# Optimization experiments

Hardware: AMD Instinct MI355X
Metric: run time of the kernel (lower is better)

Reference implementation:

```python
import jax, jax.numpy as jnp
import numpy as np

B, S, HID = 1, 2048, 2880
H, KV, D = 64, 8, 64
WINDOW = 128
SCALE = D ** -0.5
NEG_INF = jnp.float32(-1e30)


def _rope_cos_sin():
    # realistic RoPE tables over full head_dim (HF rotate_half convention)
    inv_freq = 1.0 / (10000.0 ** (np.arange(0, D, 2, dtype=np.float32) / D))
    t = np.arange(S, dtype=np.float32)
    freqs = np.outer(t, inv_freq)                      # [S, D/2]
    emb = np.concatenate([freqs, freqs], axis=-1)      # [S, D]
    return jnp.asarray(np.cos(emb))[None], jnp.asarray(np.sin(emb))[None]


def setup_inputs() -> dict:
    key = jax.random.key(0)
    ks = jax.random.split(key, 10)
    cos, sin = _rope_cos_sin()
    sd = lambda fan_in: 1.0 / np.sqrt(fan_in)
    return {
        "hidden_states": jax.random.normal(ks[0], (B, S, HID), jnp.float32),
        "cos": cos, "sin": sin,
        "Wq": jax.random.normal(ks[1], (HID, H * D), jnp.float32) * sd(HID),
        "bq": jax.random.normal(ks[2], (H * D,), jnp.float32) * 0.02,
        "Wk": jax.random.normal(ks[3], (HID, KV * D), jnp.float32) * sd(HID),
        "bk": jax.random.normal(ks[4], (KV * D,), jnp.float32) * 0.02,
        "Wv": jax.random.normal(ks[5], (HID, KV * D), jnp.float32) * sd(HID),
        "bv": jax.random.normal(ks[6], (KV * D,), jnp.float32) * 0.02,
        "Wo": jax.random.normal(ks[7], (H * D, HID), jnp.float32) * sd(H * D),
        "bo": jax.random.normal(ks[8], (HID,), jnp.float32) * 0.02,
        "sinks": jax.random.normal(ks[9], (H,), jnp.float32),
    }


def _rotate_half(x):
    x1, x2 = jnp.split(x, 2, axis=-1)
    return jnp.concatenate([-x2, x1], axis=-1)


def _forward(hidden_states, cos, sin, Wq, bq, Wk, bk, Wv, bv, Wo, bo, sinks):
    q = (hidden_states @ Wq + bq).reshape(B, S, H, D)
    k = (hidden_states @ Wk + bk).reshape(B, S, KV, D)
    v = (hidden_states @ Wv + bv).reshape(B, S, KV, D)
    # RoPE with explicit cos/sin, unsqueeze at head dim (bsnd layout)
    c, s = cos[:, :, None, :], sin[:, :, None, :]
    q = q * c + _rotate_half(q) * s
    k = k * c + _rotate_half(k) * s
    # GQA: expand kv heads to match query heads
    k = jnp.repeat(k, H // KV, axis=2)
    v = jnp.repeat(v, H // KV, axis=2)
    scores = jnp.einsum("bqhd,bkhd->bhqk", q, k) * SCALE  # [B,H,S,S]
    i = jnp.arange(S)[:, None]
    j = jnp.arange(S)[None, :]
    allowed = (j <= i) & (j > i - WINDOW)                  # causal + sliding window
    scores = jnp.where(allowed, scores, NEG_INF)
    # sink-augmented softmax: sinks act as an extra logit per head, dropped after norm
    m = jnp.maximum(scores.max(axis=-1), sinks[None, :, None])  # [B,H,S]
    p = jnp.exp(scores - m[..., None])                      # [B,H,S,S]
    denom = p.sum(axis=-1) + jnp.exp(sinks[None, :, None] - m)  # [B,H,S]
    attn = jnp.einsum("bhqk,bkhd->bqhd", p, v) / denom.transpose(0, 2, 1)[..., None]
    return attn.reshape(B, S, H * D) @ Wo + bo


def reference(hidden_states, cos, sin, Wq, bq, Wk, bk, Wv, bv, Wo, bo, sinks):
    return _forward(hidden_states, cos, sin, Wq, bq, Wk, bk, Wv, bv, Wo, bo, sinks)
```

## Files before the change

kernel.cpp:

```cpp
#include <hip/hip_runtime.h>

typedef unsigned short u16;
typedef __bf16 bf16x8 __attribute__((ext_vector_type(8)));
typedef float f32x4 __attribute__((ext_vector_type(4)));

constexpr int SEQ = 2048;
constexpr int HIDN = 2880;
constexpr int NQKV = 5120;
constexpr float SCALE = 0.125f;
constexpr float NEG_INF = -1e30f;

#define ASM_VMCNT4()  asm volatile("s_waitcnt vmcnt(4)" ::: "memory")
#define ASM_VMCNT0()  asm volatile("s_waitcnt vmcnt(0)" ::: "memory")
#define ASM_LGKM0()   asm volatile("s_waitcnt lgkmcnt(0)" ::: "memory")
#define ASM_BARRIER() asm volatile("s_barrier" ::: "memory")

__device__ __forceinline__ u16 f2bf(float f) {
  unsigned int u = __builtin_bit_cast(unsigned int, f);
  u += 0x7FFFu + ((u >> 16) & 1u);
  return (u16)(u >> 16);
}
__device__ __forceinline__ float bf2f(u16 h) {
  unsigned int u = ((unsigned int)h) << 16;
  return __builtin_bit_cast(float, u);
}
__device__ __forceinline__ void async_load16(const void* g, void* l) {
  __builtin_amdgcn_global_load_lds(
      (const __attribute__((address_space(1))) unsigned int*)g,
      (__attribute__((address_space(3))) unsigned int*)l, 16, 0, 0);
}

__global__ __launch_bounds__(256) void conv_f2b(const float* __restrict__ in,
                                                u16* __restrict__ out, long n4) {
  long i = (long)blockIdx.x * 256 + threadIdx.x;
  if (i >= n4) return;
  float4 v = ((const float4*)in)[i];
  u16 o0 = f2bf(v.x), o1 = f2bf(v.y), o2 = f2bf(v.z), o3 = f2bf(v.w);
  out[i * 4 + 0] = o0; out[i * 4 + 1] = o1; out[i * 4 + 2] = o2; out[i * 4 + 3] = o3;
}

__global__ __launch_bounds__(256) void transpose_f2b(const float* __restrict__ in,
                                                     u16* __restrict__ out,
                                                     int R, int C, int ostride) {
  __shared__ float tile[32][33];
  int c0 = blockIdx.x * 32, r0 = blockIdx.y * 32;
  int tx = threadIdx.x & 31, ty = threadIdx.x >> 5;
#pragma unroll
  for (int i = 0; i < 32; i += 8)
    tile[ty + i][tx] = in[(long)(r0 + ty + i) * C + c0 + tx];
  __syncthreads();
#pragma unroll
  for (int i = 0; i < 32; i += 8)
    out[(long)(c0 + ty + i) * ostride + r0 + tx] = f2bf(tile[tx][ty + i]);
}

__global__ __launch_bounds__(256) void concat_bias(const float* bq, const float* bk,
                                                   const float* bv, float* out) {
  int t = blockIdx.x * 256 + threadIdx.x;
  if (t < 4096) out[t] = bq[t];
  else if (t < 4608) out[t] = bk[t - 4096];
  else if (t < 5120) out[t] = bv[t - 4608];
}

template <bool OUT_BF16>
__global__ __launch_bounds__(256, 3) void gemm_pipe(const u16* __restrict__ A,
                                                    const u16* __restrict__ B,
                                                    const float* __restrict__ bias,
                                                    void* __restrict__ Cout,
                                                    int M, int N, int K) {
  __shared__ u16 As[3][128 * 32];
  __shared__ u16 Bs[3][128 * 32];
  const int tid = threadIdx.x;
  const int wid = tid >> 6, lane = tid & 63;
  const int lr = lane & 15, lk = lane >> 4;
  const int wm = wid >> 1, wn = wid & 1;

  const int gm = gridDim.x;
  int nwg = gm * gridDim.y;
  int bid = blockIdx.y * gm + blockIdx.x;
  int q8 = nwg >> 3, r8 = nwg & 7;
  int xcd = bid & 7, seq = bid >> 3;
  int swz = (xcd < r8 ? xcd * (q8 + 1) : r8 * (q8 + 1) + (xcd - r8) * q8) + seq;
  const long brow = (long)(swz % gm) * 128;
  const long bcol = (long)(swz / gm) * 128;

  const int c0 = wid * 128 + lane;
  const int c1 = c0 + 64;
  const int r0s = c0 >> 2, k0s = ((c0 & 3) ^ ((r0s >> 1) & 3)) * 8;
  const int r1s = c1 >> 2, k1s = ((c1 & 3) ^ ((r1s >> 1) & 3)) * 8;
  const u16* Asrc0 = A + (brow + r0s) * (long)K + k0s;
  const u16* Asrc1 = A + (brow + r1s) * (long)K + k1s;
  const u16* Bsrc0 = B + (bcol + r0s) * (long)K + k0s;
  const u16* Bsrc1 = B + (bcol + r1s) * (long)K + k1s;
  char* AsB = (char*)&As[0][0];
  char* BsB = (char*)&Bs[0][0];

  auto stage = [&](int kt, int bufi) {
    long ko = (long)kt * 32;
    char* la = AsB + bufi * 8192;
    char* lb = BsB + bufi * 8192;
    async_load16(Asrc0 + ko, la + c0 * 16);
    async_load16(Bsrc0 + ko, lb + c0 * 16);
    async_load16(Asrc1 + ko, la + c1 * 16);
    async_load16(Bsrc1 + ko, lb + c1 * 16);
  };

  const int phys = (lk ^ ((lr >> 1) & 3)) << 4;
  const int aoff0 = (wm * 64 + lr) * 64 + phys;
  const int boff0 = (wn * 64 + lr) * 64 + phys;

  f32x4 acc[4][4] = {};
  const int nk = K >> 5;

  stage(0, 0);
  if (nk > 1) stage(1, 1);

  int b = 0, sb = 2;
  for (int kt = 0; kt < nk; ++kt) {
    if (kt + 1 < nk) { ASM_VMCNT4(); } else { ASM_VMCNT0(); }
    ASM_BARRIER();
    __builtin_amdgcn_sched_barrier(0);
    if (kt + 2 < nk) stage(kt + 2, sb);
    char* Ab_ = AsB + b * 8192;
    char* Bb_ = BsB + b * 8192;
    bf16x8 af[4], bfr[4];
#pragma unroll
    for (int m = 0; m < 4; ++m) af[m] = *(const bf16x8*)(Ab_ + aoff0 + m * 1024);
#pragma unroll
    for (int n = 0; n < 4; ++n) bfr[n] = *(const bf16x8*)(Bb_ + boff0 + n * 1024);
    ASM_LGKM0();
    __builtin_amdgcn_sched_barrier(0);
    __builtin_amdgcn_s_setprio(1);
#pragma unroll
    for (int m = 0; m < 4; ++m)
#pragma unroll
      for (int n = 0; n < 4; ++n)
        acc[m][n] = __builtin_amdgcn_mfma_f32_16x16x32_bf16(af[m], bfr[n], acc[m][n], 0, 0, 0);
    __builtin_amdgcn_s_setprio(0);
    b = (b == 2) ? 0 : b + 1;
    sb = (sb == 2) ? 0 : sb + 1;
  }

#pragma unroll
  for (int m = 0; m < 4; ++m) {
    long row = brow + wm * 64 + m * 16 + lk * 4;
#pragma unroll
    for (int n = 0; n < 4; ++n) {
      long col = bcol + wn * 64 + n * 16 + lr;
      if (col < N) {
        float bv = bias[col];
#pragma unroll
        for (int r = 0; r < 4; ++r) {
          float v = acc[m][n][r] + bv;
          if (OUT_BF16) ((u16*)Cout)[(row + r) * (long)N + col] = f2bf(v);
          else          ((float*)Cout)[(row + r) * (long)N + col] = v;
        }
      }
    }
  }
}

__global__ __launch_bounds__(256) void rope_kernel(u16* __restrict__ QKV,
                                                   const float* __restrict__ cosb,
                                                   const float* __restrict__ sinb) {
  long idx = (long)blockIdx.x * 256 + threadIdx.x;
  if (idx >= (long)SEQ * 72 * 32) return;
  int d = idx & 31;
  int h = (int)((idx >> 5) % 72);
  int s = (int)(idx / (72 * 32));
  int col = (h < 64) ? h * 64 : 4096 + (h - 64) * 64;
  u16* p = QKV + (long)s * NQKV + col;
  float x1 = bf2f(p[d]), x2 = bf2f(p[d + 32]);
  float c = cosb[s * 64 + d], sn = sinb[s * 64 + d];
  p[d]      = f2bf(x1 * c - x2 * sn);
  p[d + 32] = f2bf(x2 * c + x1 * sn);
}

__global__ __launch_bounds__(256, 1) void attn_kernel(const u16* __restrict__ QKV,
                                                      const float* __restrict__ sinks,
                                                      u16* __restrict__ Oa) {
  __shared__ u16 Ks[64 * 64];
  __shared__ u16 Vt[64 * 64];
  __shared__ u16 Ps[4][64 * 72];
  const int tid = threadIdx.x, wid = tid >> 6, lane = tid & 63;
  const int lr = lane & 15, lk = lane >> 4;
  const int i0 = blockIdx.x * 64;
  const int h = blockIdx.y * 4 + wid;
  const int g = h >> 3;

  bf16x8 qf[4][2];
#pragma unroll
  for (int m = 0; m < 4; ++m)
#pragma unroll
    for (int kc = 0; kc < 2; ++kc)
      qf[m][kc] = *(const bf16x8*)&QKV[(long)(i0 + m * 16 + lr) * NQKV + h * 64 + kc * 32 + lk * 8];

  const float sinkh = sinks[h];
  float mrun[4][4], lrun[4][4];
  f32x4 oacc[4][4] = {};
#pragma unroll
  for (int m = 0; m < 4; ++m)
#pragma unroll
    for (int r = 0; r < 4; ++r) { mrun[m][r] = sinkh; lrun[m][r] = 0.f; }

  const int jb0 = (i0 >= 128) ? (i0 - 128) : 0;
  for (int jb = jb0; jb <= i0; jb += 64) {
#pragma unroll
    for (int i = 0; i < 2; ++i) {
      int c = wid * 128 + i * 64 + lane;
      int row = c >> 3, sp = c & 7;
      int ssrc = sp ^ (row & 7);
      async_load16(QKV + (long)(jb + row) * NQKV + 4096 + g * 64 + ssrc * 8,
                   ((char*)Ks) + c * 16);
    }
    {
      int j0 = (tid & 31) * 2, d0 = (tid >> 5) * 8;
      const u16* vp = QKV + (long)(jb + j0) * NQKV + 4608 + g * 64 + d0;
      int4 rv0 = *(const int4*)vp;
      int4 rv1 = *(const int4*)(vp + NQKV);
      const u16* a0 = (const u16*)&rv0;
      const u16* a1 = (const u16*)&rv1;
#pragma unroll
      for (int e = 0; e < 8; ++e) {
        int d = d0 + e;
        unsigned val = (unsigned)a0[e] | ((unsigned)a1[e] << 16);
        int byt = d * 128 + ((((j0 >> 3) ^ (d & 7)) << 4)) + ((j0 & 7) * 2);
        *(unsigned*)((char*)Vt + byt) = val;
      }
    }
    __syncthreads();

    f32x4 sf[4][4] = {};
    __builtin_amdgcn_s_setprio(1);
#pragma unroll
    for (int kc = 0; kc < 2; ++kc) {
      bf16x8 kf[4];
#pragma unroll
      for (int cf = 0; cf < 4; ++cf) {
        int row = cf * 16 + lr;
        kf[cf] = *(const bf16x8*)((const char*)Ks + row * 128 + (((kc * 4 + lk) ^ (lr & 7)) << 4));
      }
#pragma unroll
      for (int m = 0; m < 4; ++m)
#pragma unroll
        for (int cf = 0; cf < 4; ++cf)
          sf[m][cf] = __builtin_amdgcn_mfma_f32_16x16x32_bf16(qf[m][kc], kf[cf], sf[m][cf], 0, 0, 0);
    }
    __builtin_amdgcn_s_setprio(0);

#pragma unroll
    for (int m = 0; m < 4; ++m) {
      float rmax[4];
#pragma unroll
      for (int r = 0; r < 4; ++r) {
        int i = i0 + m * 16 + lk * 4 + r;
        float mx = NEG_INF;
#pragma unroll
        for (int cf = 0; cf < 4; ++cf) {
          int j = jb + cf * 16 + lr;
          float v = sf[m][cf][r] * SCALE;
          bool ok = (j <= i) && (j > i - 128);
          v = ok ? v : NEG_INF;
          sf[m][cf][r] = v;
          mx = fmaxf(mx, v);
        }
#pragma unroll
        for (int off = 1; off < 16; off <<= 1) mx = fmaxf(mx, __shfl_xor(mx, off, 64));
        rmax[r] = mx;
      }
#pragma unroll
      for (int r = 0; r < 4; ++r) {
        float mnew = fmaxf(mrun[m][r], rmax[r]);
        float corr = __expf(mrun[m][r] - mnew);
        mrun[m][r] = mnew;
        float rsum = 0.f;
#pragma unroll
        for (int cf = 0; cf < 4; ++cf) {
          float p = __expf(sf[m][cf][r] - mnew);
          sf[m][cf][r] = p;
          rsum += p;
        }
#pragma unroll
        for (int off = 1; off < 16; off <<= 1) rsum += __shfl_xor(rsum, off, 64);
        lrun[m][r] = lrun[m][r] * corr + rsum;
#pragma unroll
        for (int dn = 0; dn < 4; ++dn) oacc[m][dn][r] *= corr;
      }
    }

#pragma unroll
    for (int m = 0; m < 4; ++m)
#pragma unroll
      for (int cf = 0; cf < 4; ++cf)
#pragma unroll
        for (int r = 0; r < 4; ++r)
          Ps[wid][(m * 16 + lk * 4 + r) * 72 + cf * 16 + lr] = f2bf(sf[m][cf][r]);
    __syncthreads();

    __builtin_amdgcn_s_setprio(1);
#pragma unroll
    for (int kc = 0; kc < 2; ++kc) {
      bf16x8 pf[4], vf[4];
#pragma unroll
      for (int m = 0; m < 4; ++m)
        pf[m] = *(const bf16x8*)&Ps[wid][(m * 16 + lr) * 72 + kc * 32 + lk * 8];
#pragma unroll
      for (int dn = 0; dn < 4; ++dn) {
        int row = dn * 16 + lr;
        vf[dn] = *(const bf16x8*)((const char*)Vt + row * 128 + (((kc * 4 + lk) ^ (lr & 7)) << 4));
      }
#pragma unroll
      for (int m = 0; m < 4; ++m)
#pragma unroll
        for (int dn = 0; dn < 4; ++dn)
          oacc[m][dn] = __builtin_amdgcn_mfma_f32_16x16x32_bf16(pf[m], vf[dn], oacc[m][dn], 0, 0, 0);
    }
    __builtin_amdgcn_s_setprio(0);
    __syncthreads();
  }

#pragma unroll
  for (int m = 0; m < 4; ++m)
#pragma unroll
    for (int r = 0; r < 4; ++r) {
      float denom = lrun[m][r] + __expf(sinkh - mrun[m][r]);
      float inv = 1.f / denom;
      long row = i0 + m * 16 + lk * 4 + r;
#pragma unroll
      for (int dn = 0; dn < 4; ++dn)
        Oa[row * 4096 + h * 64 + dn * 16 + lr] = f2bf(oacc[m][dn][r] * inv);
    }
}

extern "C" void kernel_launch(void* const* d_in, const int* in_sizes, int n_in,
                              void* d_out, int out_size, void* d_ws, size_t ws_size,
                              hipStream_t stream) {
  const float* X    = (const float*)d_in[0];
  const float* cosb = (const float*)d_in[1];
  const float* sinb = (const float*)d_in[2];
  const float* Wq   = (const float*)d_in[3];
  const float* bq   = (const float*)d_in[4];
  const float* Wk   = (const float*)d_in[5];
  const float* bk   = (const float*)d_in[6];
  const float* Wv   = (const float*)d_in[7];
  const float* bv   = (const float*)d_in[8];
  const float* Wo   = (const float*)d_in[9];
  const float* bo   = (const float*)d_in[10];
  const float* sinks = (const float*)d_in[11];

  char* ws = (char*)d_ws;
  size_t off = 0;
  auto alloc = [&](size_t bytes) -> void* {
    void* p = ws + off;
    off += (bytes + 255) & ~(size_t)255;
    return p;
  };
  u16*   Xb    = (u16*)alloc((size_t)SEQ * HIDN * 2);
  u16*   Wqkv  = (u16*)alloc((size_t)NQKV * HIDN * 2);
  u16*   Wot   = (u16*)alloc((size_t)2944 * 4096 * 2);
  float* bqkv  = (float*)alloc((size_t)NQKV * 4);
  u16*   QKV   = (u16*)alloc((size_t)SEQ * NQKV * 2);
  u16*   Ab    = (u16*)alloc((size_t)SEQ * 4096 * 2);
  (void)ws_size; (void)in_sizes; (void)n_in; (void)out_size;

  conv_f2b<<<(SEQ * HIDN / 4 + 255) / 256, 256, 0, stream>>>(X, Xb, (long)SEQ * HIDN / 4);
  transpose_f2b<<<dim3(4096 / 32, HIDN / 32), 256, 0, stream>>>(Wq, Wqkv, HIDN, 4096, HIDN);
  transpose_f2b<<<dim3(512 / 32, HIDN / 32), 256, 0, stream>>>(Wk, Wqkv + (size_t)4096 * HIDN, HIDN, 512, HIDN);
  transpose_f2b<<<dim3(512 / 32, HIDN / 32), 256, 0, stream>>>(Wv, Wqkv + (size_t)4608 * HIDN, HIDN, 512, HIDN);
  transpose_f2b<<<dim3(HIDN / 32, 4096 / 32), 256, 0, stream>>>(Wo, Wot, 4096, HIDN, 4096);
  concat_bias<<<(NQKV + 255) / 256, 256, 0, stream>>>(bq, bk, bv, bqkv);
  gemm_pipe<true><<<dim3(SEQ / 128, NQKV / 128), 256, 0, stream>>>(Xb, Wqkv, bqkv, QKV, SEQ, NQKV, HIDN);
  rope_kernel<<<(int)(((long)SEQ * 72 * 32 + 255) / 256), 256, 0, stream>>>(QKV, cosb, sinb);
  attn_kernel<<<dim3(SEQ / 64, 64 / 4), 256, 0, stream>>>(QKV, sinks, Ab);
  gemm_pipe<false><<<dim3(SEQ / 128, (HIDN + 127) / 128), 256, 0, stream>>>(Ab, Wot, bo, d_out, SEQ, HIDN, 4096);
}
```

Before: 259.7 us.

## Replace GEMMs with larger 512-thread tiles and deeper LDS pipelining

Replaces the generic 128x128 GEMM with two specialized kernels. The QKV projection gets a 256x256 tile over 8 waves, with A fragments split into two halves to overlap LDS reads and MFMA. The output projection gets a 128x256 tile with a 4-stage prefetch ring. Hand-written ds_read_b128 is used, and the XOR swizzle on LDS is dropped, which may cause bank conflicts. The Wo transpose buffer is padded to 3072 columns so the tiles cover it.

After: 248.8 us. 4.2% less time.

```diff
diff --git a/kernel.cpp b/kernel.cpp
--- a/kernel.cpp
+++ b/kernel.cpp
@@ -10,10 +10,10 @@
 constexpr float SCALE = 0.125f;
 constexpr float NEG_INF = -1e30f;
 
-#define ASM_VMCNT4()  asm volatile("s_waitcnt vmcnt(4)" ::: "memory")
-#define ASM_VMCNT0()  asm volatile("s_waitcnt vmcnt(0)" ::: "memory")
+#define ASM_VMCNT(n)  asm volatile("s_waitcnt vmcnt(" #n ")" ::: "memory")
 #define ASM_LGKM0()   asm volatile("s_waitcnt lgkmcnt(0)" ::: "memory")
 #define ASM_BARRIER() asm volatile("s_barrier" ::: "memory")
+#define SCHEDBAR()    __builtin_amdgcn_sched_barrier(0)
 
 __device__ __forceinline__ u16 f2bf(float f) {
   unsigned int u = __builtin_bit_cast(unsigned int, f);
@@ -29,6 +29,12 @@
       (const __attribute__((address_space(1))) unsigned int*)g,
       (__attribute__((address_space(3))) unsigned int*)l, 16, 0, 0);
 }
+__device__ __forceinline__ f32x4 DSR(unsigned addr) {
+  f32x4 d;
+  asm volatile("ds_read_b128 %0, %1" : "=v"(d) : "v"(addr));
+  return d;
+}
+__device__ __forceinline__ bf16x8 asbf(f32x4 v) { return __builtin_bit_cast(bf16x8, v); }
 
 __global__ __launch_bounds__(256) void conv_f2b(const float* __restrict__ in,
                                                 u16* __restrict__ out, long n4) {
@@ -62,18 +68,109 @@
   else if (t < 5120) out[t] = bv[t - 4608];
 }
 
-template <bool OUT_BF16>
-__global__ __launch_bounds__(256, 3) void gemm_pipe(const u16* __restrict__ A,
-                                                    const u16* __restrict__ B,
-                                                    const float* __restrict__ bias,
-                                                    void* __restrict__ Cout,
-                                                    int M, int N, int K) {
-  __shared__ u16 As[3][128 * 32];
-  __shared__ u16 Bs[3][128 * 32];
-  const int tid = threadIdx.x;
-  const int wid = tid >> 6, lane = tid & 63;
+__global__ __launch_bounds__(512, 2) void gemm256(const u16* __restrict__ A,
+                                                  const u16* __restrict__ B,
+                                                  const float* __restrict__ bias,
+                                                  u16* __restrict__ C,
+                                                  int N, int K) {
+  __shared__ u16 lds[3 * 16384];
+  const int tid = threadIdx.x, wid = tid >> 6, lane = tid & 63;
   const int lr = lane & 15, lk = lane >> 4;
-  const int wm = wid >> 1, wn = wid & 1;
+  const int wm = wid >> 2, wn = wid & 3;
+
+  const int gm = gridDim.x;
+  int nwg = gm * gridDim.y;
+  int bid = blockIdx.y * gm + blockIdx.x;
+  int q8 = nwg >> 3, r8 = nwg & 7;
+  int xcd = bid & 7, seq = bid >> 3;
+  int swz = (xcd < r8 ? xcd * (q8 + 1) : r8 * (q8 + 1) + (xcd - r8) * q8) + seq;
+  const long brow = (long)(swz % gm) * 256;
+  const long bcol = (long)(swz / gm) * 256;
+  const int nkt = K >> 5;
+
+  const int cA0 = tid, cA1 = tid + 512;
+  const u16* Asrc0 = A + (brow + (cA0 >> 2)) * (long)K + (cA0 & 3) * 8;
+  const u16* Asrc1 = A + (brow + (cA1 >> 2)) * (long)K + (cA1 & 3) * 8;
+  const u16* Bsrc0 = B + (bcol + (cA0 >> 2)) * (long)K + (cA0 & 3) * 8;
+  const u16* Bsrc1 = B + (bcol + (cA1 >> 2)) * (long)K + (cA1 & 3) * 8;
+  char* L = (char*)lds;
+  auto stage = [&](int kt, int b) {
+    long ko = (long)kt * 32;
+    char* d = L + b * 32768;
+    async_load16(Asrc0 + ko, d + cA0 * 16);
+    async_load16(Asrc1 + ko, d + cA1 * 16);
+    async_load16(Bsrc0 + ko, d + 16384 + cA0 * 16);
+    async_load16(Bsrc1 + ko, d + 16384 + cA1 * 16);
+  };
+
+  const unsigned lds0 = (unsigned)(size_t)L;
+  const unsigned aoff = lds0 + (unsigned)((wm * 128 + lr) * 64 + lk * 16);
+  const unsigned boff = lds0 + 16384u + (unsigned)((wn * 64 + lr) * 64 + lk * 16);
+
+  f32x4 acc[8][4] = {};
+  stage(0, 0);
+  stage(1, 1);
+  ASM_VMCNT(4);
+  ASM_BARRIER();
+
+  int b = 0;
+  for (int t = 0; t < nkt; ++t) {
+    const unsigned ab = aoff + b * 32768u;
+    const unsigned bb = boff + b * 32768u;
+    f32x4 afr[4], bfr[4];
+#pragma unroll
+    for (int m = 0; m < 4; ++m) afr[m] = DSR(ab + m * 1024u);
+#pragma unroll
+    for (int n = 0; n < 4; ++n) bfr[n] = DSR(bb + n * 1024u);
+    if (t + 2 < nkt) stage(t + 2, b == 0 ? 2 : b - 1);
+    ASM_LGKM0(); SCHEDBAR();
+    __builtin_amdgcn_s_setprio(1);
+#pragma unroll
+    for (int m = 0; m < 4; ++m)
+#pragma unroll
+      for (int n = 0; n < 4; ++n)
+        acc[m][n] = __builtin_amdgcn_mfma_f32_16x16x32_bf16(asbf(afr[m]), asbf(bfr[n]), acc[m][n], 0, 0, 0);
+    __builtin_amdgcn_s_setprio(0);
+    f32x4 afr2[4];
+#pragma unroll
+    for (int m = 0; m < 4; ++m) afr2[m] = DSR(ab + (m + 4) * 1024u);
+    if (t + 2 < nkt) { ASM_VMCNT(4); } else { ASM_VMCNT(0); }
+    ASM_BARRIER();
+    ASM_LGKM0(); SCHEDBAR();
+    __builtin_amdgcn_s_setprio(1);
+#pragma unroll
+    for (int m = 0; m < 4; ++m)
+#pragma unroll
+      for (int n = 0; n < 4; ++n)
+        acc[m + 4][n] = __builtin_amdgcn_mfma_f32_16x16x32_bf16(asbf(afr2[m]), asbf(bfr[n]), acc[m + 4][n], 0, 0, 0);
+    __builtin_amdgcn_s_setprio(0);
+    ASM_BARRIER();
+    b = (b == 2) ? 0 : b + 1;
+  }
+
+#pragma unroll
+  for (int m = 0; m < 8; ++m) {
+    long row = brow + wm * 128 + m * 16 + lk * 4;
+#pragma unroll
+    for (int n = 0; n < 4; ++n) {
+      long col = bcol + wn * 64 + n * 16 + lr;
+      float bv = bias[col];
+#pragma unroll
+      for (int r = 0; r < 4; ++r)
+        C[(row + r) * (long)N + col] = f2bf(acc[m][n][r] + bv);
+    }
+  }
+}
+
+__global__ __launch_bounds__(512, 2) void gemm128(const u16* __restrict__ A,
+                                                  const u16* __restrict__ B,
+                                                  const float* __restrict__ bias,
+                                                  float* __restrict__ C,
+                                                  int N, int K) {
+  __shared__ u16 lds[4 * 12288];
+  const int tid = threadIdx.x, wid = tid >> 6, lane = tid & 63;
+  const int lr = lane & 15, lk = lane >> 4;
+  const int wm = wid >> 2, wn = wid & 3;
 
   const int gm = gridDim.x;
   int nwg = gm * gridDim.y;
@@ -82,63 +179,56 @@
   int xcd = bid & 7, seq = bid >> 3;
   int swz = (xcd < r8 ? xcd * (q8 + 1) : r8 * (q8 + 1) + (xcd - r8) * q8) + seq;
   const long brow = (long)(swz % gm) * 128;
-  const long bcol = (long)(swz / gm) * 128;
-
-  const int c0 = wid * 128 + lane;
-  const int c1 = c0 + 64;
-  const int r0s = c0 >> 2, k0s = ((c0 & 3) ^ ((r0s >> 1) & 3)) * 8;
-  const int r1s = c1 >> 2, k1s = ((c1 & 3) ^ ((r1s >> 1) & 3)) * 8;
-  const u16* Asrc0 = A + (brow + r0s) * (long)K + k0s;
-  const u16* Asrc1 = A + (brow + r1s) * (long)K + k1s;
-  const u16* Bsrc0 = B + (bcol + r0s) * (long)K + k0s;
-  const u16* Bsrc1 = B + (bcol + r1s) * (long)K + k1s;
-  char* AsB = (char*)&As[0][0];
-  char* BsB = (char*)&Bs[0][0];
-
-  auto stage = [&](int kt, int bufi) {
+  const long bcol = (long)(swz / gm) * 256;
+  const int nkt = K >> 5;
+
+  const int cB0 = tid, cB1 = tid + 512;
+  const u16* AsrcP = A + (brow + (tid >> 2)) * (long)K + (tid & 3) * 8;
+  const u16* Bsrc0 = B + (bcol + (cB0 >> 2)) * (long)K + (cB0 & 3) * 8;
+  const u16* Bsrc1 = B + (bcol + (cB1 >> 2)) * (long)K + (cB1 & 3) * 8;
+  char* L = (char*)lds;
+  auto stage = [&](int kt, int b) {
     long ko = (long)kt * 32;
-    char* la = AsB + bufi * 8192;
-    char* lb = BsB + bufi * 8192;
-    async_load16(Asrc0 + ko, la + c0 * 16);
-    async_load16(Bsrc0 + ko, lb + c0 * 16);
-    async_load16(Asrc1 + ko, la + c1 * 16);
-    async_load16(Bsrc1 + ko, lb + c1 * 16);
+    char* d = L + b * 24576;
+    async_load16(AsrcP + ko, d + tid * 16);
+    async_load16(Bsrc0 + ko, d + 8192 + cB0 * 16);
+    async_load16(Bsrc1 + ko, d + 8192 + cB1 * 16);
   };
 
-  const int phys = (lk ^ ((lr >> 1) & 3)) << 4;
-  const int aoff0 = (wm * 64 + lr) * 64 + phys;
-  const int boff0 = (wn * 64 + lr) * 64 + phys;
+  const unsigned lds0 = (unsigned)(size_t)L;
+  const unsigned aoff = lds0 + (unsigned)((wm * 64 + lr) * 64 + lk * 16);
+  const unsigned boff = lds0 + 8192u + (unsigned)((wn * 64 + lr) * 64 + lk * 16);
 
   f32x4 acc[4][4] = {};
-  const int nk = K >> 5;
-
   stage(0, 0);
-  if (nk > 1) stage(1, 1);
-
-  int b = 0, sb = 2;
-  for (int kt = 0; kt < nk; ++kt) {
-    if (kt + 1 < nk) { ASM_VMCNT4(); } else { ASM_VMCNT0(); }
+  stage(1, 1);
+  stage(2, 2);
+  ASM_VMCNT(6);
+  ASM_BARRIER();
+
+  for (int t = 0; t < nkt; ++t) {
+    const int b = t & 3;
+    const unsigned ab = aoff + b * 24576u;
+    const unsigned bb = boff + b * 24576u;
+    f32x4 afr[4], bfr[4];
+#pragma unroll
+    for (int m = 0; m < 4; ++m) afr[m] = DSR(ab + m * 1024u);
+#pragma unroll
+    for (int n = 0; n < 4; ++n) bfr[n] = DSR(bb + n * 1024u);
+    if (t + 3 < nkt) stage(t + 3, (t + 3) & 3);
+    if (t + 3 < nkt)      { ASM_VMCNT(6); }
+    else if (t + 2 < nkt) { ASM_VMCNT(3); }
+    else                  { ASM_VMCNT(0); }
     ASM_BARRIER();
-    __builtin_amdgcn_sched_barrier(0);
-    if (kt + 2 < nk) stage(kt + 2, sb);
-    char* Ab_ = AsB + b * 8192;
-    char* Bb_ = BsB + b * 8192;
-    bf16x8 af[4], bfr[4];
-#pragma unroll
-    for (int m = 0; m < 4; ++m) af[m] = *(const bf16x8*)(Ab_ + aoff0 + m * 1024);
-#pragma unroll
-    for (int n = 0; n < 4; ++n) bfr[n] = *(const bf16x8*)(Bb_ + boff0 + n * 1024);
-    ASM_LGKM0();
-    __builtin_amdgcn_sched_barrier(0);
+    ASM_LGKM0(); SCHEDBAR();
     __builtin_amdgcn_s_setprio(1);
 #pragma unroll
     for (int m = 0; m < 4; ++m)
 #pragma unroll
       for (int n = 0; n < 4; ++n)
-        acc[m][n] = __builtin_amdgcn_mfma_f32_16x16x32_bf16(af[m], bfr[n], acc[m][n], 0, 0, 0);
+        acc[m][n] = __builtin_amdgcn_mfma_f32_16x16x32_bf16(asbf(afr[m]), asbf(bfr[n]), acc[m][n], 0, 0, 0);
     __builtin_amdgcn_s_setprio(0);
-    b = (b == 2) ? 0 : b + 1;
-    sb = (sb == 2) ? 0 : sb + 1;
+    ASM_BARRIER();
   }
 
 #pragma unroll
@@ -150,11 +240,8 @@
       if (col < N) {
         float bv = bias[col];
 #pragma unroll
-        for (int r = 0; r < 4; ++r) {
-          float v = acc[m][n][r] + bv;
-          if (OUT_BF16) ((u16*)Cout)[(row + r) * (long)N + col] = f2bf(v);
-          else          ((float*)Cout)[(row + r) * (long)N + col] = v;
-        }
+        for (int r = 0; r < 4; ++r)
+          C[(row + r) * (long)N + col] = acc[m][n][r] + bv;
       }
     }
   }
@@ -357,7 +444,7 @@
   };
   u16*   Xb    = (u16*)alloc((size_t)SEQ * HIDN * 2);
   u16*   Wqkv  = (u16*)alloc((size_t)NQKV * HIDN * 2);
-  u16*   Wot   = (u16*)alloc((size_t)2944 * 4096 * 2);
+  u16*   Wot   = (u16*)alloc((size_t)3072 * 4096 * 2);
   float* bqkv  = (float*)alloc((size_t)NQKV * 4);
   u16*   QKV   = (u16*)alloc((size_t)SEQ * NQKV * 2);
   u16*   Ab    = (u16*)alloc((size_t)SEQ * 4096 * 2);
@@ -369,8 +456,8 @@
   transpose_f2b<<<dim3(512 / 32, HIDN / 32), 256, 0, stream>>>(Wv, Wqkv + (size_t)4608 * HIDN, HIDN, 512, HIDN);
   transpose_f2b<<<dim3(HIDN / 32, 4096 / 32), 256, 0, stream>>>(Wo, Wot, 4096, HIDN, 4096);
   concat_bias<<<(NQKV + 255) / 256, 256, 0, stream>>>(bq, bk, bv, bqkv);
-  gemm_pipe<true><<<dim3(SEQ / 128, NQKV / 128), 256, 0, stream>>>(Xb, Wqkv, bqkv, QKV, SEQ, NQKV, HIDN);
+  gemm256<<<dim3(SEQ / 256, NQKV / 256), 512, 0, stream>>>(Xb, Wqkv, bqkv, QKV, NQKV, HIDN);
   rope_kernel<<<(int)(((long)SEQ * 72 * 32 + 255) / 256), 256, 0, stream>>>(QKV, cosb, sinb);
   attn_kernel<<<dim3(SEQ / 64, 64 / 4), 256, 0, stream>>>(QKV, sinks, Ab);
-  gemm_pipe<false><<<dim3(SEQ / 128, (HIDN + 127) / 128), 256, 0, stream>>>(Ab, Wot, bo, d_out, SEQ, HIDN, 4096);
-}
+  gemm128<<<dim3(SEQ / 128, 3072 / 256), 512, 0, stream>>>(Ab, Wot, bo, (float*)d_out, HIDN, 4096);
+}
```

## Widen GEMM tiles to 128x256 with split LDS reads and MFMA halves

Applied to the files above, without the earlier changes.

Replaces the 128x128 GEMM with a 128x256 tile kernel in which each of the four waves owns a 128x64 slice. That doubles the A-fragment reuse per B fragment and cuts redundant A traffic. The LDS fragment reads are issued as inline ds_read_b128 and split in two, so the first half of the MFMAs can start under a partial lgkmcnt wait while the rest of the reads complete. The output-projection weight buffer is padded to 3072 rows to fit the wider tile, and the stores stay guarded by col<N. The cost is fewer workgroups (192–320 on a 256-CU part), lower occupancy (2 blocks per CU instead of 3) and more LDS per block, which may leave CUs underused.

Measured after the change: 262.7 us. No clear change (+1.1%).

```diff
diff --git a/kernel.cpp b/kernel.cpp
--- a/kernel.cpp
+++ b/kernel.cpp
@@ -10,10 +10,10 @@
 constexpr float SCALE = 0.125f;
 constexpr float NEG_INF = -1e30f;
 
-#define ASM_VMCNT4()  asm volatile("s_waitcnt vmcnt(4)" ::: "memory")
-#define ASM_VMCNT0()  asm volatile("s_waitcnt vmcnt(0)" ::: "memory")
-#define ASM_LGKM0()   asm volatile("s_waitcnt lgkmcnt(0)" ::: "memory")
+#define ASM_VMCNT(n)  asm volatile("s_waitcnt vmcnt(" #n ")" ::: "memory")
+#define ASM_LGKM(n)   asm volatile("s_waitcnt lgkmcnt(" #n ")" ::: "memory")
 #define ASM_BARRIER() asm volatile("s_barrier" ::: "memory")
+#define SCHEDBAR()    __builtin_amdgcn_sched_barrier(0)
 
 __device__ __forceinline__ u16 f2bf(float f) {
   unsigned int u = __builtin_bit_cast(unsigned int, f);
@@ -29,6 +29,12 @@
       (const __attribute__((address_space(1))) unsigned int*)g,
       (__attribute__((address_space(3))) unsigned int*)l, 16, 0, 0);
 }
+__device__ __forceinline__ f32x4 DSR(unsigned addr) {
+  f32x4 d;
+  asm volatile("ds_read_b128 %0, %1" : "=v"(d) : "v"(addr));
+  return d;
+}
+__device__ __forceinline__ bf16x8 asbf(f32x4 v) { return __builtin_bit_cast(bf16x8, v); }
 
 __global__ __launch_bounds__(256) void conv_f2b(const float* __restrict__ in,
                                                 u16* __restrict__ out, long n4) {
@@ -63,17 +69,14 @@
 }
 
 template <bool OUT_BF16>
-__global__ __launch_bounds__(256, 3) void gemm_pipe(const u16* __restrict__ A,
-                                                    const u16* __restrict__ B,
-                                                    const float* __restrict__ bias,
-                                                    void* __restrict__ Cout,
-                                                    int M, int N, int K) {
-  __shared__ u16 As[3][128 * 32];
-  __shared__ u16 Bs[3][128 * 32];
-  const int tid = threadIdx.x;
-  const int wid = tid >> 6, lane = tid & 63;
+__global__ __launch_bounds__(256, 2) void gemm_kb(const u16* __restrict__ A,
+                                                  const u16* __restrict__ B,
+                                                  const float* __restrict__ bias,
+                                                  void* __restrict__ Cout,
+                                                  int N, int K) {
+  __shared__ u16 lds[3 * 12288];
+  const int tid = threadIdx.x, lane = tid & 63, wn = tid >> 6;
   const int lr = lane & 15, lk = lane >> 4;
-  const int wm = wid >> 1, wn = wid & 1;
 
   const int gm = gridDim.x;
   int nwg = gm * gridDim.y;
@@ -82,68 +85,78 @@
   int xcd = bid & 7, seq = bid >> 3;
   int swz = (xcd < r8 ? xcd * (q8 + 1) : r8 * (q8 + 1) + (xcd - r8) * q8) + seq;
   const long brow = (long)(swz % gm) * 128;
-  const long bcol = (long)(swz / gm) * 128;
-
-  const int c0 = wid * 128 + lane;
-  const int c1 = c0 + 64;
-  const int r0s = c0 >> 2, k0s = ((c0 & 3) ^ ((r0s >> 1) & 3)) * 8;
-  const int r1s = c1 >> 2, k1s = ((c1 & 3) ^ ((r1s >> 1) & 3)) * 8;
-  const u16* Asrc0 = A + (brow + r0s) * (long)K + k0s;
-  const u16* Asrc1 = A + (brow + r1s) * (long)K + k1s;
-  const u16* Bsrc0 = B + (bcol + r0s) * (long)K + k0s;
-  const u16* Bsrc1 = B + (bcol + r1s) * (long)K + k1s;
-  char* AsB = (char*)&As[0][0];
-  char* BsB = (char*)&Bs[0][0];
-
-  auto stage = [&](int kt, int bufi) {
+  const long bcol = (long)(swz / gm) * 256;
+  const int nkt = K >> 5;
+
+  const int ca0 = tid, ca1 = tid + 256;
+  const u16* As0 = A + (brow + (ca0 >> 2)) * (long)K + ((ca0 & 3) ^ ((ca0 >> 3) & 3)) * 8;
+  const u16* As1 = A + (brow + (ca1 >> 2)) * (long)K + ((ca1 & 3) ^ ((ca1 >> 3) & 3)) * 8;
+  const u16* Bsr[4];
+#pragma unroll
+  for (int i = 0; i < 4; ++i) {
+    int c = tid + 256 * i;
+    Bsr[i] = B + (bcol + (c >> 2)) * (long)K + ((c & 3) ^ ((c >> 3) & 3)) * 8;
+  }
+  char* L = (char*)lds;
+  auto stage = [&](int kt, int b) {
     long ko = (long)kt * 32;
-    char* la = AsB + bufi * 8192;
-    char* lb = BsB + bufi * 8192;
-    async_load16(Asrc0 + ko, la + c0 * 16);
-    async_load16(Bsrc0 + ko, lb + c0 * 16);
-    async_load16(Asrc1 + ko, la + c1 * 16);
-    async_load16(Bsrc1 + ko, lb + c1 * 16);
+    char* d = L + b * 24576;
+    async_load16(As0 + ko, d + ca0 * 16);
+    async_load16(As1 + ko, d + ca1 * 16);
+#pragma unroll
+    for (int i = 0; i < 4; ++i)
+      async_load16(Bsr[i] + ko, d + 8192 + (tid + 256 * i) * 16);
   };
 
-  const int phys = (lk ^ ((lr >> 1) & 3)) << 4;
-  const int aoff0 = (wm * 64 + lr) * 64 + phys;
-  const int boff0 = (wn * 64 + lr) * 64 + phys;
-
-  f32x4 acc[4][4] = {};
-  const int nk = K >> 5;
-
+  const unsigned lds0 = (unsigned)(size_t)L;
+  const unsigned xs = (unsigned)((lk ^ ((lr >> 1) & 3)) << 4);
+  const unsigned aoff = lds0 + (unsigned)(lr * 64) + xs;
+  const unsigned boff = lds0 + 8192u + (unsigned)((wn * 64 + lr) * 64) + xs;
+
+  f32x4 acc[8][4] = {};
   stage(0, 0);
-  if (nk > 1) stage(1, 1);
+  if (nkt > 1) stage(1, 1);
 
   int b = 0, sb = 2;
-  for (int kt = 0; kt < nk; ++kt) {
-    if (kt + 1 < nk) { ASM_VMCNT4(); } else { ASM_VMCNT0(); }
+  for (int t = 0; t < nkt; ++t) {
+    if (t + 2 < nkt)      { stage(t + 2, sb); ASM_VMCNT(12); }
+    else if (t + 1 < nkt) { ASM_VMCNT(6); }
+    else                  { ASM_VMCNT(0); }
     ASM_BARRIER();
-    __builtin_amdgcn_sched_barrier(0);
-    if (kt + 2 < nk) stage(kt + 2, sb);
-    char* Ab_ = AsB + b * 8192;
-    char* Bb_ = BsB + b * 8192;
-    bf16x8 af[4], bfr[4];
-#pragma unroll
-    for (int m = 0; m < 4; ++m) af[m] = *(const bf16x8*)(Ab_ + aoff0 + m * 1024);
-#pragma unroll
-    for (int n = 0; n < 4; ++n) bfr[n] = *(const bf16x8*)(Bb_ + boff0 + n * 1024);
-    ASM_LGKM0();
-    __builtin_amdgcn_sched_barrier(0);
+
+    const unsigned ab = aoff + (unsigned)(b * 24576);
+    const unsigned bb = boff + (unsigned)(b * 24576);
+    f32x4 af[8], bf4[4];
+#pragma unroll
+    for (int m = 0; m < 4; ++m) af[m] = DSR(ab + m * 1024u);
+#pragma unroll
+    for (int n = 0; n < 4; ++n) bf4[n] = DSR(bb + n * 1024u);
+#pragma unroll
+    for (int m = 4; m < 8; ++m) af[m] = DSR(ab + m * 1024u);
+    ASM_LGKM(4); SCHEDBAR();
     __builtin_amdgcn_s_setprio(1);
 #pragma unroll
     for (int m = 0; m < 4; ++m)
 #pragma unroll
       for (int n = 0; n < 4; ++n)
-        acc[m][n] = __builtin_amdgcn_mfma_f32_16x16x32_bf16(af[m], bfr[n], acc[m][n], 0, 0, 0);
+        acc[m][n] = __builtin_amdgcn_mfma_f32_16x16x32_bf16(asbf(af[m]), asbf(bf4[n]), acc[m][n], 0, 0, 0);
     __builtin_amdgcn_s_setprio(0);
+    ASM_LGKM(0); SCHEDBAR();
+    __builtin_amdgcn_s_setprio(1);
+#pragma unroll
+    for (int m = 4; m < 8; ++m)
+#pragma unroll
+      for (int n = 0; n < 4; ++n)
+        acc[m][n] = __builtin_amdgcn_mfma_f32_16x16x32_bf16(asbf(af[m]), asbf(bf4[n]), acc[m][n], 0, 0, 0);
+    __builtin_amdgcn_s_setprio(0);
+    ASM_BARRIER();
     b = (b == 2) ? 0 : b + 1;
     sb = (sb == 2) ? 0 : sb + 1;
   }
 
 #pragma unroll
-  for (int m = 0; m < 4; ++m) {
-    long row = brow + wm * 64 + m * 16 + lk * 4;
+  for (int m = 0; m < 8; ++m) {
+    long row = brow + m * 16 + lk * 4;
 #pragma unroll
     for (int n = 0; n < 4; ++n) {
       long col = bcol + wn * 64 + n * 16 + lr;
@@ -357,7 +370,7 @@
   };
   u16*   Xb    = (u16*)alloc((size_t)SEQ * HIDN * 2);
   u16*   Wqkv  = (u16*)alloc((size_t)NQKV * HIDN * 2);
-  u16*   Wot   = (u16*)alloc((size_t)2944 * 4096 * 2);
+  u16*   Wot   = (u16*)alloc((size_t)3072 * 4096 * 2);
   float* bqkv  = (float*)alloc((size_t)NQKV * 4);
   u16*   QKV   = (u16*)alloc((size_t)SEQ * NQKV * 2);
   u16*   Ab    = (u16*)alloc((size_t)SEQ * 4096 * 2);
@@ -369,8 +382,8 @@
   transpose_f2b<<<dim3(512 / 32, HIDN / 32), 256, 0, stream>>>(Wv, Wqkv + (size_t)4608 * HIDN, HIDN, 512, HIDN);
   transpose_f2b<<<dim3(HIDN / 32, 4096 / 32), 256, 0, stream>>>(Wo, Wot, 4096, HIDN, 4096);
   concat_bias<<<(NQKV + 255) / 256, 256, 0, stream>>>(bq, bk, bv, bqkv);
-  gemm_pipe<true><<<dim3(SEQ / 128, NQKV / 128), 256, 0, stream>>>(Xb, Wqkv, bqkv, QKV, SEQ, NQKV, HIDN);
+  gemm_kb<true><<<dim3(SEQ / 128, NQKV / 256), 256, 0, stream>>>(Xb, Wqkv, bqkv, QKV, NQKV, HIDN);
   rope_kernel<<<(int)(((long)SEQ * 72 * 32 + 255) / 256), 256, 0, stream>>>(QKV, cosb, sinb);
   attn_kernel<<<dim3(SEQ / 64, 64 / 4), 256, 0, stream>>>(QKV, sinks, Ab);
-  gemm_pipe<false><<<dim3(SEQ / 128, (HIDN + 127) / 128), 256, 0, stream>>>(Ab, Wot, bo, d_out, SEQ, HIDN, 4096);
-}
+  gemm_kb<false><<<dim3(SEQ / 128, 3072 / 256), 256, 0, stream>>>(Ab, Wot, bo, (float*)d_out, HIDN, 4096);
+}
```
